# Optimization experiments

Measured on AMD Instinct MI355X. Metric: run time of the kernel, lower is better.

The kernel has to match this reference:

```python
import jax, jax.numpy as jnp
import numpy as np

N_NODES = 50000
N_EDGES = 800000
DIMS = [128, 512, 256, 128]
EPS = 1e-5


def setup_inputs() -> dict:
    key = jax.random.key(0)
    ks = jax.random.split(key, 2 + 5 * 3)
    inp = {
        "x": jax.random.normal(ks[0], (N_NODES, DIMS[0]), dtype=jnp.float32),
        "edge_index": jax.random.randint(ks[1], (2, N_EDGES), 0, N_NODES, dtype=jnp.int64),
    }
    ki = 2
    for i in range(3):
        din, dout = DIMS[i], DIMS[i + 1]
        s = 1.0 / np.sqrt(din)
        inp[f"Wl{i}"] = jax.random.uniform(ks[ki + 0], (din, dout), jnp.float32, -s, s)
        inp[f"bl{i}"] = jax.random.uniform(ks[ki + 1], (dout,), jnp.float32, -s, s)
        inp[f"Wr{i}"] = jax.random.uniform(ks[ki + 2], (din, dout), jnp.float32, -s, s)
        inp[f"g{i}"] = jnp.ones((dout,), jnp.float32)
        inp[f"b{i}"] = jnp.zeros((dout,), jnp.float32)
        ki += 5
    return inp


def _sage_mean(x, src, dst, Wl, bl, Wr):
    n = x.shape[0]
    agg = jax.ops.segment_sum(x[src], dst, num_segments=n)  # [N, din]
    deg = jax.ops.segment_sum(jnp.ones((src.shape[0],), x.dtype), dst, num_segments=n)
    mean = agg / jnp.maximum(deg, 1.0)[:, None]
    return mean @ Wl + bl + x @ Wr


def _bn(h, gamma, beta):
    m = h.mean(axis=0)
    v = h.var(axis=0)
    return gamma * (h - m) * jax.lax.rsqrt(v + EPS) + beta


def reference(x, edge_index, Wl0, bl0, Wr0, g0, b0, Wl1, bl1, Wr1, g1, b1, Wl2, bl2, Wr2, g2, b2):
    src, dst = edge_index[0], edge_index[1]
    params = [(Wl0, bl0, Wr0, g0, b0), (Wl1, bl1, Wr1, g1, b1), (Wl2, bl2, Wr2, g2, b2)]
    h = x
    for Wl, bl, Wr, g, b in params:
        h = _sage_mean(h, src, dst, Wl, bl, Wr)
        h = _bn(h, g, b)
        h = jax.nn.relu(h)
        # dropout: identity in eval mode
    return h
```

## Files before the change

### kernel.cpp

```cpp
#include <hip/hip_runtime.h>
#include <cstdint>
#include <cstddef>


#define EPS_BN 1e-5f

typedef unsigned short ushort_t;
typedef __attribute__((ext_vector_type(8))) short short8;
typedef __attribute__((ext_vector_type(4))) float float4v;
typedef __attribute__((ext_vector_type(2))) float float2v;
typedef __attribute__((ext_vector_type(2))) unsigned int uint2v;
typedef __attribute__((ext_vector_type(4))) unsigned int uint4v;

__device__ __forceinline__ float bflo(unsigned int w) {
    union { unsigned int i; float f; } v; v.i = w << 16; return v.f;
}
__device__ __forceinline__ float bfhi(unsigned int w) {
    union { unsigned int i; float f; } v; v.i = w & 0xffff0000u; return v.f;
}
__device__ __forceinline__ ushort_t f2bf(float f) {
    union { float f; unsigned int i; } v; v.f = f;
    unsigned int r = v.i + 0x7fffu + ((v.i >> 16) & 1u);
    return (ushort_t)(r >> 16);
}

__device__ __forceinline__ void async_copy16(void* lds, const void* g) {
    __builtin_amdgcn_global_load_lds(
        (const __attribute__((address_space(1))) unsigned int*)g,
        (__attribute__((address_space(3))) unsigned int*)lds, 16, 0, 0);
}

__device__ __forceinline__ void edge_sd(const int* __restrict__ p, int e, int ne,
                                        bool is64, int& s, int& d) {
    if (is64) { s = p[2 * e];  d = p[2 * ne + 2 * e]; }
    else      { s = p[e];      d = p[ne + e]; }
}
__device__ __forceinline__ int edge_d(const int* __restrict__ p, int e, int ne, bool is64) {
    return is64 ? p[2 * ne + 2 * e] : p[ne + e];
}

__device__ __forceinline__ bool detect_is64(const int* __restrict__ edges,
                                            int* sh_flag, int t) {
    if (t == 0) *sh_flag = 1;
    __syncthreads();
    if (t < 64 && edges[2 * t + 1] != 0) *sh_flag = 0;
    __syncthreads();
    return *sh_flag != 0;
}

#define EPB 2048

__global__ __launch_bounds__(256) void bhist_kernel(
    const int* __restrict__ edges, int ne, int* __restrict__ gcnt) {
    __shared__ int h[256];
    __shared__ int f64;
    int t = threadIdx.x;
    bool is64 = detect_is64(edges, &f64, t);
    h[t] = 0;
    __syncthreads();
    int base_e = blockIdx.x * EPB;
    #pragma unroll
    for (int u = 0; u < EPB / 256; ++u) {
        int i = base_e + u * 256 + t;
        if (i < ne) atomicAdd(&h[edge_d(edges, i, ne, is64) >> 8], 1);
    }
    __syncthreads();
    if (h[t]) atomicAdd(&gcnt[t], h[t]);
}

__global__ __launch_bounds__(256) void bscan_kernel(
    const int* __restrict__ gcnt, int nb, int ne,
    int* __restrict__ bbase, int* __restrict__ bcur) {
    __shared__ int sh[256];
    int t = threadIdx.x;
    int v = (t < nb) ? gcnt[t] : 0;
    sh[t] = v;
    __syncthreads();
    for (int o = 1; o < 256; o <<= 1) {
        int x = (t >= o) ? sh[t - o] : 0;
        __syncthreads();
        sh[t] += x;
        __syncthreads();
    }
    int excl = sh[t] - v;
    if (t < nb) { bbase[t] = excl; bcur[t] = excl; }
    if (t == nb) bbase[t] = ne;
    if (t == 0 && nb == 256) bbase[256] = ne;
}

__global__ __launch_bounds__(256) void bscatter_kernel(
    const int* __restrict__ edges, int ne,
    int* __restrict__ bcur, int* __restrict__ packed) {
    __shared__ int h[256];
    __shared__ int chunkb[256];
    __shared__ int lcur[256];
    __shared__ int f64;
    int t = threadIdx.x;
    bool is64 = detect_is64(edges, &f64, t);
    h[t] = 0;
    lcur[t] = 0;
    __syncthreads();
    int base_e = blockIdx.x * EPB;
    int ent[EPB / 256], eb[EPB / 256];
    #pragma unroll
    for (int u = 0; u < EPB / 256; ++u) {
        int i = base_e + u * 256 + t;
        if (i < ne) {
            int s, d;
            edge_sd(edges, i, ne, is64, s, d);
            ent[u] = s | ((d & 255) << 24);
            eb[u] = d >> 8;
            atomicAdd(&h[eb[u]], 1);
        } else eb[u] = -1;
    }
    __syncthreads();
    if (h[t]) chunkb[t] = atomicAdd(&bcur[t], h[t]);
    __syncthreads();
    #pragma unroll
    for (int u = 0; u < EPB / 256; ++u) {
        if (eb[u] >= 0) {
            int lp = atomicAdd(&lcur[eb[u]], 1);
            packed[chunkb[eb[u]] + lp] = ent[u];
        }
    }
}

__global__ __launch_bounds__(256) void bbuild_kernel(
    const int* __restrict__ packed, const int* __restrict__ bbase,
    int* __restrict__ rowptr, int* __restrict__ csr_src, int n) {
    __shared__ int h[256];
    __shared__ int cur[256];
    int t = threadIdx.x;
    int bb = blockIdx.x;
    int base = bbase[bb], cnt = bbase[bb + 1] - base;
    h[t] = 0;
    __syncthreads();
    for (int i = t; i < cnt; i += 256)
        atomicAdd(&h[(unsigned)packed[base + i] >> 24], 1);
    __syncthreads();
    int v = h[t];
    for (int o = 1; o < 256; o <<= 1) {
        int x = (t >= o) ? h[t - o] : 0;
        __syncthreads();
        h[t] += x;
        __syncthreads();
    }
    int excl = h[t] - v;
    int node = bb * 256 + t;
    if (node <= n) rowptr[node] = base + excl;
    cur[t] = excl;
    __syncthreads();
    for (int i = t; i < cnt; i += 256) {
        int e = packed[base + i];
        int lp = atomicAdd(&cur[(unsigned)e >> 24], 1);
        csr_src[base + lp] = e & 0xffffff;
    }
}

__global__ void prep_all_kernel(
    const float* __restrict__ x, ushort_t* __restrict__ xb, int nxb,
    const float* __restrict__ Wl0, const float* __restrict__ Wr0,
    ushort_t* __restrict__ WT0, int nb0,
    const float* __restrict__ Wl1, const float* __restrict__ Wr1,
    ushort_t* __restrict__ WT1c, int nb1,
    const float* __restrict__ Wl2, const float* __restrict__ Wr2,
    ushort_t* __restrict__ WT2c) {
    const int D0 = 128, D1 = 512, D2 = 256, D3 = 128;
    int b = blockIdx.x;
    if (b < nxb) {
        int i = b * 256 + threadIdx.x;
        xb[i] = f2bf(x[i]);
        return;
    }
    b -= nxb;
    if (b < nb0) {
        int idx = b * 256 + threadIdx.x;
        int K2 = 2 * D0;
        int nn = idx / K2, k = idx - nn * K2;
        float v = (k < D0) ? Wl0[(size_t)k * D1 + nn] : Wr0[(size_t)(k - D0) * D1 + nn];
        WT0[idx] = f2bf(v);
        return;
    }
    b -= nb0;
    if (b < nb1) {
        int idx = b * 256 + threadIdx.x;
        int nn = idx / D1, k = idx - nn * D1;
        float v = (nn < D2) ? Wl1[(size_t)k * D2 + nn] : Wr1[(size_t)k * D2 + (nn - D2)];
        WT1c[idx] = f2bf(v);
        return;
    }
    b -= nb1;
    {
        int idx = b * 256 + threadIdx.x;
        int nn = idx / D2, k = idx - nn * D2;
        float v = (nn < D3) ? Wl2[(size_t)k * D3 + nn] : Wr2[(size_t)k * D3 + (nn - D3)];
        WT2c[idx] = f2bf(v);
    }
}

template <int VEC> struct VecT;
template <> struct VecT<2> { using T = unsigned int; };
template <> struct VecT<4> { using T = uint2v; };
template <> struct VecT<8> { using T = uint4v; };

template <int VEC>
__device__ __forceinline__ void vunpack(typename VecT<VEC>::T v, unsigned int* w) {
    if constexpr (VEC == 2) { w[0] = v; }
    else if constexpr (VEC == 4) { w[0] = v.x; w[1] = v.y; }
    else { w[0] = v.x; w[1] = v.y; w[2] = v.z; w[3] = v.w; }
}

template <int VEC>
__device__ __forceinline__ void vaccum(typename VecT<VEC>::T v, float* acc) {
    unsigned int w[VEC / 2];
    vunpack<VEC>(v, w);
    #pragma unroll
    for (int i = 0; i < VEC / 2; ++i) {
        acc[2 * i + 0] += bflo(w[i]);
        acc[2 * i + 1] += bfhi(w[i]);
    }
}

template <int VEC>
__device__ __forceinline__ void gather_sum(
    const ushort_t* __restrict__ base, const int* __restrict__ csr_src,
    int e0, int e1, int rstride, float* acc) {
    using VT = typename VecT<VEC>::T;
    int e = e0;
    for (; e + 16 <= e1; e += 16) {
        VT v[16];
        #pragma unroll
        for (int u = 0; u < 16; ++u)
            v[u] = *(const VT*)(base + (size_t)csr_src[e + u] * rstride);
        #pragma unroll
        for (int u = 0; u < 16; ++u) vaccum<VEC>(v[u], acc);
    }
    if (e + 8 <= e1) {
        VT v[8];
        #pragma unroll
        for (int u = 0; u < 8; ++u)
            v[u] = *(const VT*)(base + (size_t)csr_src[e + u] * rstride);
        #pragma unroll
        for (int u = 0; u < 8; ++u) vaccum<VEC>(v[u], acc);
        e += 8;
    }
    if (e + 4 <= e1) {
        VT v[4];
        #pragma unroll
        for (int u = 0; u < 4; ++u)
            v[u] = *(const VT*)(base + (size_t)csr_src[e + u] * rstride);
        #pragma unroll
        for (int u = 0; u < 4; ++u) vaccum<VEC>(v[u], acc);
        e += 4;
    }
    if (e + 2 <= e1) {
        VT v0 = *(const VT*)(base + (size_t)csr_src[e] * rstride);
        VT v1 = *(const VT*)(base + (size_t)csr_src[e + 1] * rstride);
        vaccum<VEC>(v0, acc); vaccum<VEC>(v1, acc);
        e += 2;
    }
    if (e < e1)
        vaccum<VEC>(*(const VT*)(base + (size_t)csr_src[e] * rstride), acc);
}

template <int VEC>
__global__ __launch_bounds__(256) void aggregate_wave_kernel(
    const ushort_t* __restrict__ h, ushort_t* __restrict__ mean,
    const int* __restrict__ rowptr, const int* __restrict__ csr_src, int nnodes) {
    const int din = VEC * 64;
    const int wave = threadIdx.x >> 6;
    const int lane = threadIdx.x & 63;
    const int wstride = gridDim.x * 4;
    using VT = typename VecT<VEC>::T;
    for (int wid = blockIdx.x * 4 + wave; wid < nnodes; wid += wstride) {
        int e0 = rowptr[wid], e1 = rowptr[wid + 1];
        float acc[VEC];
        #pragma unroll
        for (int i = 0; i < VEC; ++i) acc[i] = 0.f;
        gather_sum<VEC>(h + (size_t)lane * VEC, csr_src, e0, e1, din, acc);

        int deg = e1 - e0;
        float scale = 1.0f / (float)(deg > 1 ? deg : 1);
        unsigned int o[VEC / 2];
        #pragma unroll
        for (int i = 0; i < VEC / 2; ++i)
            o[i] = (unsigned int)f2bf(acc[2 * i] * scale) |
                   ((unsigned int)f2bf(acc[2 * i + 1] * scale) << 16);
        VT ov;
        if constexpr (VEC == 2) { ov = o[0]; }
        else if constexpr (VEC == 4) { ov.x = o[0]; ov.y = o[1]; }
        else { ov.x = o[0]; ov.y = o[1]; ov.z = o[2]; ov.w = o[3]; }
        *(VT*)(mean + (size_t)wid * din + (size_t)lane * VEC) = ov;
    }
}

template <int VEC>
__global__ __launch_bounds__(256) void aggregate_add_kernel(
    const ushort_t* __restrict__ PR, const float* __restrict__ bias,
    ushort_t* __restrict__ pre,
    const int* __restrict__ rowptr, const int* __restrict__ csr_src, int nnodes,
    float* __restrict__ gsum, float* __restrict__ gsq) {
    const int D = VEC * 64;
    const int stride = 2 * D;
    __shared__ float s_red[2][4][VEC * 64];
    const int wave = threadIdx.x >> 6;
    const int lane = threadIdx.x & 63;
    const int wstride = gridDim.x * 4;
    using VT = typename VecT<VEC>::T;

    float ssum[VEC], ssq[VEC];
    #pragma unroll
    for (int i = 0; i < VEC; ++i) { ssum[i] = 0.f; ssq[i] = 0.f; }

    for (int wid = blockIdx.x * 4 + wave; wid < nnodes; wid += wstride) {
        int e0 = rowptr[wid], e1 = rowptr[wid + 1];
        float acc[VEC];
        #pragma unroll
        for (int i = 0; i < VEC; ++i) acc[i] = 0.f;
        gather_sum<VEC>(PR + (size_t)lane * VEC, csr_src, e0, e1, stride, acc);

        int deg = e1 - e0;
        float scale = 1.0f / (float)(deg > 1 ? deg : 1);

        VT rv = *(const VT*)(PR + (size_t)wid * stride + D + (size_t)lane * VEC);
        unsigned int rw[VEC / 2];
        vunpack<VEC>(rv, rw);
        float o[VEC];
        #pragma unroll
        for (int i = 0; i < VEC / 2; ++i) {
            o[2 * i + 0] = bflo(rw[i]);
            o[2 * i + 1] = bfhi(rw[i]);
        }
        #pragma unroll
        for (int i = 0; i < VEC; ++i) {
            o[i] += acc[i] * scale + bias[lane * VEC + i];
            ssum[i] += o[i];
            ssq[i] += o[i] * o[i];
        }

        unsigned int ow[VEC / 2];
        #pragma unroll
        for (int i = 0; i < VEC / 2; ++i)
            ow[i] = (unsigned int)f2bf(o[2 * i]) | ((unsigned int)f2bf(o[2 * i + 1]) << 16);
        VT ov;
        if constexpr (VEC == 2) { ov = ow[0]; }
        else if constexpr (VEC == 4) { ov.x = ow[0]; ov.y = ow[1]; }
        else { ov.x = ow[0]; ov.y = ow[1]; ov.z = ow[2]; ov.w = ow[3]; }
        *(VT*)(pre + (size_t)wid * D + (size_t)lane * VEC) = ov;
    }

    #pragma unroll
    for (int i = 0; i < VEC; ++i) {
        s_red[0][wave][lane * VEC + i] = ssum[i];
        s_red[1][wave][lane * VEC + i] = ssq[i];
    }
    __syncthreads();
    int t = threadIdx.x;
    if (t < D) {
        float a = s_red[0][0][t] + s_red[0][1][t] + s_red[0][2][t] + s_red[0][3][t];
        float q = s_red[1][0][t] + s_red[1][1][t] + s_red[1][2][t] + s_red[1][3][t];
        atomicAdd(&gsum[t], a);
        atomicAdd(&gsq[t], q);
    }
}

template <int K, int COLS, bool DUAL, bool BIAS, bool STATS>
__global__ __launch_bounds__(256, 2) void gemm_bres_kernel(
    const ushort_t* __restrict__ A1, const ushort_t* __restrict__ A2,
    const ushort_t* __restrict__ BT, const float* __restrict__ bias,
    ushort_t* __restrict__ Cb, int N, int nRowTiles, int RG, int panelsLog2,
    int Wtot, float* __restrict__ gsum, float* __restrict__ gsq) {
    __shared__ ushort_t Bs[COLS * K];

    const int tid = threadIdx.x;
    const int wave = tid >> 6;
    const int lane = tid & 63;
    const int quad = lane >> 4;
    const int l15 = lane & 15;

    const int nwg = gridDim.x;
    const int q = nwg >> 3, rr = nwg & 7;
    const int o = blockIdx.x;
    const int xcd = o & 7, sub = o >> 3;
    const int wgid = (xcd < rr ? xcd * (q + 1) : rr * (q + 1) + (xcd - rr) * q) + sub;
    const int panel = wgid & ((1 << panelsLog2) - 1);
    const int rowGroup = wgid >> panelsLog2;
    const int colBase = panel * COLS;

    constexpr int CPC = K / 8;
    constexpr int CPT = COLS * CPC / 256;
    #pragma unroll
    for (int u = 0; u < CPT; ++u) {
        int c = u * 256 + tid;
        int col = c / CPC, cc = c - col * CPC;
        int scc = cc ^ (col & 7);
        async_copy16(&Bs[c * 8], BT + (size_t)(colBase + col) * K + scc * 8);
    }
    __syncthreads();

    const int wm = (wave >> 1) * 64;
    constexpr int WN = COLS / 2;
    const int wn = (wave & 1) * WN;
    constexpr int NJ = WN / 16;
    constexpr int NKK = K / 32;
    constexpr int AS = DUAL ? K / 2 : K;

    float cs[NJ][4], cq[NJ][4];
    if constexpr (STATS) {
        #pragma unroll
        for (int j = 0; j < NJ; ++j)
            #pragma unroll
            for (int r = 0; r < 4; ++r) { cs[j][r] = 0.f; cq[j][r] = 0.f; }
    }

    for (int rt = rowGroup; rt < nRowTiles; rt += RG) {
        const int rowBase = rt * 128;
        const ushort_t* ap[4];
        const ushort_t* ap2[4];
        int growv[4];
        #pragma unroll
        for (int i = 0; i < 4; ++i) {
            int grow = rowBase + wm + i * 16 + l15;
            growv[i] = grow;
            if (grow >= N) grow = N - 1;
            ap[i] = A1 + (size_t)grow * AS + quad * 8;
            if (DUAL) ap2[i] = A2 + (size_t)grow * AS + quad * 8;
        }

        float4v acc[4][NJ];
        #pragma unroll
        for (int i = 0; i < 4; ++i)
            #pragma unroll
            for (int j = 0; j < NJ; ++j)
                acc[i][j] = (float4v){0.f, 0.f, 0.f, 0.f};

        #pragma unroll
        for (int kk = 0; kk < NKK; ++kk) {
            short8 af[4], bf[NJ];
            #pragma unroll
            for (int i = 0; i < 4; ++i) {
                if constexpr (DUAL) {
                    if (kk < NKK / 2) af[i] = *(const short8*)(ap[i] + kk * 32);
                    else              af[i] = *(const short8*)(ap2[i] + (kk - NKK / 2) * 32);
                } else {
                    af[i] = *(const short8*)(ap[i] + kk * 32);
                }
            }
            #pragma unroll
            for (int j = 0; j < NJ; ++j) {
                int col = wn + j * 16 + l15;
                int ct = (kk * 4 + quad) ^ (col & 7);
                bf[j] = *(const short8*)&Bs[col * K + ct * 8];
            }
            __builtin_amdgcn_s_setprio(1);
            #pragma unroll
            for (int i = 0; i < 4; ++i)
                #pragma unroll
                for (int j = 0; j < NJ; ++j)
                    acc[i][j] = __builtin_amdgcn_mfma_f32_16x16x32_bf16(bf[j], af[i], acc[i][j], 0, 0, 0);
            __builtin_amdgcn_s_setprio(0);
        }

        #pragma unroll
        for (int j = 0; j < NJ; ++j) {
            float4 bv = make_float4(0.f, 0.f, 0.f, 0.f);
            if (BIAS) bv = *(const float4*)(bias + colBase + wn + j * 16 + quad * 4);
            #pragma unroll
            for (int i = 0; i < 4; ++i) {
                float v0 = acc[i][j][0] + bv.x;
                float v1 = acc[i][j][1] + bv.y;
                float v2 = acc[i][j][2] + bv.z;
                float v3 = acc[i][j][3] + bv.w;
                if (growv[i] < N) {
                    if constexpr (STATS) {
                        cs[j][0] += v0; cq[j][0] += v0 * v0;
                        cs[j][1] += v1; cq[j][1] += v1 * v1;
                        cs[j][2] += v2; cq[j][2] += v2 * v2;
                        cs[j][3] += v3; cq[j][3] += v3 * v3;
                    }
                    uint2v pk;
                    pk.x = (unsigned int)f2bf(v0) | ((unsigned int)f2bf(v1) << 16);
                    pk.y = (unsigned int)f2bf(v2) | ((unsigned int)f2bf(v3) << 16);
                    *(uint2v*)(Cb + (size_t)growv[i] * Wtot + colBase + wn + j * 16 + quad * 4) = pk;
                }
            }
        }
    }

    if constexpr (STATS) {
        #pragma unroll
        for (int j = 0; j < NJ; ++j)
            #pragma unroll
            for (int r = 0; r < 4; ++r) {
                #pragma unroll
                for (int m = 1; m < 16; m <<= 1) {
                    cs[j][r] += __shfl_xor(cs[j][r], m);
                    cq[j][r] += __shfl_xor(cq[j][r], m);
                }
            }
        if (l15 == 0) {
            #pragma unroll
            for (int j = 0; j < NJ; ++j)
                #pragma unroll
                for (int r = 0; r < 4; ++r) {
                    int col = colBase + wn + j * 16 + quad * 4 + r;
                    atomicAdd(&gsum[col], cs[j][r]);
                    atomicAdd(&gsq[col], cq[j][r]);
                }
        }
    }
}

__global__ void bn_relu_b2b_kernel(const ushort_t* __restrict__ h, ushort_t* __restrict__ hb,
                                   int N, int D,
                                   const float* __restrict__ sum, const float* __restrict__ sumsq,
                                   const float* __restrict__ g, const float* __restrict__ b) {
    size_t idx = (size_t)blockIdx.x * blockDim.x + threadIdx.x;
    size_t tot = (size_t)N * D / 2;
    if (idx >= tot) return;
    int cp = (int)(idx & (size_t)(D / 2 - 1));
    int c0 = cp * 2, c1 = c0 + 1;
    float m0 = sum[c0] / (float)N, m1 = sum[c1] / (float)N;
    float i0 = rsqrtf(sumsq[c0] / (float)N - m0 * m0 + EPS_BN);
    float i1 = rsqrtf(sumsq[c1] / (float)N - m1 * m1 + EPS_BN);
    unsigned int w = ((const unsigned int*)h)[idx];
    float v0 = g[c0] * (bflo(w) - m0) * i0 + b[c0];
    float v1 = g[c1] * (bfhi(w) - m1) * i1 + b[c1];
    v0 = v0 > 0.f ? v0 : 0.f;
    v1 = v1 > 0.f ? v1 : 0.f;
    ((unsigned int*)hb)[idx] = (unsigned int)f2bf(v0) | ((unsigned int)f2bf(v1) << 16);
}

__global__ void bn_relu_b2f_kernel(const ushort_t* __restrict__ h, float* __restrict__ hf,
                                   int N, int D,
                                   const float* __restrict__ sum, const float* __restrict__ sumsq,
                                   const float* __restrict__ g, const float* __restrict__ b) {
    size_t idx = (size_t)blockIdx.x * blockDim.x + threadIdx.x;
    size_t tot = (size_t)N * D / 2;
    if (idx >= tot) return;
    int cp = (int)(idx & (size_t)(D / 2 - 1));
    int c0 = cp * 2, c1 = c0 + 1;
    float m0 = sum[c0] / (float)N, m1 = sum[c1] / (float)N;
    float i0 = rsqrtf(sumsq[c0] / (float)N - m0 * m0 + EPS_BN);
    float i1 = rsqrtf(sumsq[c1] / (float)N - m1 * m1 + EPS_BN);
    unsigned int w = ((const unsigned int*)h)[idx];
    float v0 = g[c0] * (bflo(w) - m0) * i0 + b[c0];
    float v1 = g[c1] * (bfhi(w) - m1) * i1 + b[c1];
    float2v o;
    o.x = v0 > 0.f ? v0 : 0.f;
    o.y = v1 > 0.f ? v1 : 0.f;
    *(float2v*)(hf + idx * 2) = o;
}

extern "C" void kernel_launch(void* const* d_in, const int* in_sizes, int n_in,
                              void* d_out, int out_size, void* d_ws, size_t ws_size,
                              hipStream_t stream) {
    const float* x     = (const float*)d_in[0];
    const int*   edges = (const int*)d_in[1];
    const float* Wl0 = (const float*)d_in[2];
    const float* bl0 = (const float*)d_in[3];
    const float* Wr0 = (const float*)d_in[4];
    const float* g0  = (const float*)d_in[5];
    const float* b0  = (const float*)d_in[6];
    const float* Wl1 = (const float*)d_in[7];
    const float* bl1 = (const float*)d_in[8];
    const float* Wr1 = (const float*)d_in[9];
    const float* g1  = (const float*)d_in[10];
    const float* b1  = (const float*)d_in[11];
    const float* Wl2 = (const float*)d_in[12];
    const float* bl2 = (const float*)d_in[13];
    const float* Wr2 = (const float*)d_in[14];
    const float* g2  = (const float*)d_in[15];
    const float* b2  = (const float*)d_in[16];

    const int D0 = 128, D1 = 512, D2 = 256, D3 = 128;
    const int n  = in_sizes[0] / D0;
    const int ne = in_sizes[1] / 2;
    const int NB = (n + 255) >> 8;

    char* base = (char*)d_ws;
    size_t off = 0;
    auto alloc = [&](size_t bytes) -> char* {
        char* p = base + off;
        off = (off + bytes + 255) & ~(size_t)255;
        return p;
    };
    int*      gcnt    = (int*)alloc(256 * 4);
    float*    stats   = (float*)alloc(6 * 512 * 4);
    size_t    zero_span = off;
    int*      bbase   = (int*)alloc(257 * 4);
    int*      bcur    = (int*)alloc(256 * 4);
    int*      packed  = (int*)alloc((size_t)ne * 4);
    int*      rowptr  = (int*)alloc((size_t)(n + 1) * 4);
    int*      csr_src = (int*)alloc((size_t)ne * 4);
    ushort_t* xb      = (ushort_t*)alloc((size_t)n * D0 * 2);
    ushort_t* mb      = (ushort_t*)alloc((size_t)n * 512 * 2);
    ushort_t* h1b     = (ushort_t*)alloc((size_t)n * D1 * 2);
    ushort_t* h2b     = (ushort_t*)alloc((size_t)n * D2 * 2);
    ushort_t* hpre    = (ushort_t*)alloc((size_t)n * 512 * 2);
    ushort_t* WT0     = (ushort_t*)alloc((size_t)D1 * 2 * D0 * 2);
    ushort_t* WT1c    = (ushort_t*)alloc((size_t)(2 * D2) * D1 * 2);
    ushort_t* WT2c    = (ushort_t*)alloc((size_t)(2 * D3) * D2 * 2);
    float*    out     = (float*)d_out;
    (void)ws_size; (void)n_in; (void)out_size;

    hipMemsetAsync(base, 0, zero_span, stream);

    int ablk = (ne + EPB - 1) / EPB;
    bhist_kernel<<<ablk, 256, 0, stream>>>(edges, ne, gcnt);
    bscan_kernel<<<1, 256, 0, stream>>>(gcnt, NB, ne, bbase, bcur);
    bscatter_kernel<<<ablk, 256, 0, stream>>>(edges, ne, bcur, packed);
    bbuild_kernel<<<NB, 256, 0, stream>>>(packed, bbase, rowptr, csr_src, n);

    const int nxb = (n * D0) / 256;
    const int nb0 = (D1 * 2 * D0) / 256;
    const int nb1 = (2 * D2 * D1) / 256;
    const int nb2 = (2 * D3 * D2) / 256;
    prep_all_kernel<<<nxb + nb0 + nb1 + nb2, 256, 0, stream>>>(
        x, xb, nxb, Wl0, Wr0, WT0, nb0, Wl1, Wr1, WT1c, nb1, Wl2, Wr2, WT2c);

    const int aggGrid = 2048;
    const int rowTiles = (n + 127) / 128;
    float* st0 = stats + 0 * 1024;
    float* st1 = stats + 1 * 1024;
    float* st2 = stats + 2 * 1024;

    aggregate_wave_kernel<2><<<aggGrid, 256, 0, stream>>>(xb, mb, rowptr, csr_src, n);
    gemm_bres_kernel<256, 128, true, true, true><<<512, 256, 0, stream>>>(
        mb, xb, WT0, bl0, hpre, n, rowTiles, 128, 2, D1, st0, st0 + 512);
    bn_relu_b2b_kernel<<<((size_t)n * D1 / 2 + 255) / 256, 256, 0, stream>>>(
        hpre, h1b, n, D1, st0, st0 + 512, g0, b0);

    gemm_bres_kernel<512, 64, false, false, false><<<512, 256, 0, stream>>>(
        h1b, nullptr, WT1c, nullptr, mb, n, rowTiles, 64, 3, 2 * D2, nullptr, nullptr);
    aggregate_add_kernel<4><<<aggGrid, 256, 0, stream>>>(
        mb, bl1, hpre, rowptr, csr_src, n, st1, st1 + 512);
    bn_relu_b2b_kernel<<<((size_t)n * D2 / 2 + 255) / 256, 256, 0, stream>>>(
        hpre, h2b, n, D2, st1, st1 + 512, g1, b1);

    gemm_bres_kernel<256, 128, false, false, false><<<512, 256, 0, stream>>>(
        h2b, nullptr, WT2c, nullptr, mb, n, rowTiles, 256, 1, 2 * D3, nullptr, nullptr);
    aggregate_add_kernel<2><<<aggGrid, 256, 0, stream>>>(
        mb, bl2, hpre, rowptr, csr_src, n, st2, st2 + 512);
    bn_relu_b2f_kernel<<<((size_t)n * D3 / 2 + 255) / 256, 256, 0, stream>>>(
        hpre, out, n, D3, st2, st2 + 512, g2, b2);
}
```

Before: 604.7 us.

## Retile bf16 GEMM into 512-thread blocks with 32x32 per-wave tiles

Reworks the GEMM so each of 8 waves computes a 32x32 output tile. Column panels become narrower (32 or 64 columns) and row tiles become 128 or 256 rows. Grids grow to roughly 800-1000 workgroups with launch bounds asking for 6 blocks per CU, and the s_setprio hints around the MFMA block are removed. The aim is more parallelism and occupancy with a smaller LDS footprint per block. The cost is less register-level reuse per wave, and A rows are re-read from global memory once per extra column panel.

```diff
diff --git a/kernel.cpp b/kernel.cpp
--- a/kernel.cpp
+++ b/kernel.cpp
@@ -364,12 +364,14 @@
     }
 }
 
-template <int K, int COLS, bool DUAL, bool BIAS, bool STATS>
-__global__ __launch_bounds__(256, 2) void gemm_bres_kernel(
+template <int K, int ROWW, int COLW, bool DUAL, bool BIAS, bool STATS>
+__global__ __launch_bounds__(512, 6) void gemm_bres_kernel(
     const ushort_t* __restrict__ A1, const ushort_t* __restrict__ A2,
     const ushort_t* __restrict__ BT, const float* __restrict__ bias,
     ushort_t* __restrict__ Cb, int N, int nRowTiles, int RG, int panelsLog2,
     int Wtot, float* __restrict__ gsum, float* __restrict__ gsq) {
+    constexpr int COLS = COLW * 32;
+    constexpr int BR = ROWW * 32;
     __shared__ ushort_t Bs[COLS * K];
 
     const int tid = threadIdx.x;
@@ -377,6 +379,8 @@
     const int lane = tid & 63;
     const int quad = lane >> 4;
     const int l15 = lane & 15;
+    const int wr = wave / COLW;
+    const int wc = wave % COLW;
 
     const int nwg = gridDim.x;
     const int q = nwg >> 3, rr = nwg & 7;
@@ -388,57 +392,53 @@
     const int colBase = panel * COLS;
 
     constexpr int CPC = K / 8;
-    constexpr int CPT = COLS * CPC / 256;
+    constexpr int CPT = COLS * CPC / 512;
     #pragma unroll
     for (int u = 0; u < CPT; ++u) {
-        int c = u * 256 + tid;
+        int c = u * 512 + tid;
         int col = c / CPC, cc = c - col * CPC;
         int scc = cc ^ (col & 7);
         async_copy16(&Bs[c * 8], BT + (size_t)(colBase + col) * K + scc * 8);
     }
     __syncthreads();
 
-    const int wm = (wave >> 1) * 64;
-    constexpr int WN = COLS / 2;
-    const int wn = (wave & 1) * WN;
-    constexpr int NJ = WN / 16;
     constexpr int NKK = K / 32;
     constexpr int AS = DUAL ? K / 2 : K;
 
-    float cs[NJ][4], cq[NJ][4];
+    float cs[2][4], cq[2][4];
     if constexpr (STATS) {
         #pragma unroll
-        for (int j = 0; j < NJ; ++j)
+        for (int j = 0; j < 2; ++j)
             #pragma unroll
             for (int r = 0; r < 4; ++r) { cs[j][r] = 0.f; cq[j][r] = 0.f; }
     }
 
     for (int rt = rowGroup; rt < nRowTiles; rt += RG) {
-        const int rowBase = rt * 128;
-        const ushort_t* ap[4];
-        const ushort_t* ap2[4];
-        int growv[4];
-        #pragma unroll
-        for (int i = 0; i < 4; ++i) {
-            int grow = rowBase + wm + i * 16 + l15;
+        const int rowBase = rt * BR;
+        const ushort_t* ap[2];
+        const ushort_t* ap2[2];
+        int growv[2];
+        #pragma unroll
+        for (int i = 0; i < 2; ++i) {
+            int grow = rowBase + wr * 32 + i * 16 + l15;
             growv[i] = grow;
             if (grow >= N) grow = N - 1;
             ap[i] = A1 + (size_t)grow * AS + quad * 8;
             if (DUAL) ap2[i] = A2 + (size_t)grow * AS + quad * 8;
         }
 
-        float4v acc[4][NJ];
-        #pragma unroll
-        for (int i = 0; i < 4; ++i)
-            #pragma unroll
-            for (int j = 0; j < NJ; ++j)
+        float4v acc[2][2];
+        #pragma unroll
+        for (int i = 0; i < 2; ++i)
+            #pragma unroll
+            for (int j = 0; j < 2; ++j)
                 acc[i][j] = (float4v){0.f, 0.f, 0.f, 0.f};
 
         #pragma unroll
         for (int kk = 0; kk < NKK; ++kk) {
-            short8 af[4], bf[NJ];
-            #pragma unroll
-            for (int i = 0; i < 4; ++i) {
+            short8 af[2], bf[2];
+            #pragma unroll
+            for (int i = 0; i < 2; ++i) {
                 if constexpr (DUAL) {
                     if (kk < NKK / 2) af[i] = *(const short8*)(ap[i] + kk * 32);
                     else              af[i] = *(const short8*)(ap2[i] + (kk - NKK / 2) * 32);
@@ -447,26 +447,24 @@
                 }
             }
             #pragma unroll
-            for (int j = 0; j < NJ; ++j) {
-                int col = wn + j * 16 + l15;
+            for (int j = 0; j < 2; ++j) {
+                int col = wc * 32 + j * 16 + l15;
                 int ct = (kk * 4 + quad) ^ (col & 7);
                 bf[j] = *(const short8*)&Bs[col * K + ct * 8];
             }
-            __builtin_amdgcn_s_setprio(1);
-            #pragma unroll
-            for (int i = 0; i < 4; ++i)
+            #pragma unroll
+            for (int i = 0; i < 2; ++i)
                 #pragma unroll
-                for (int j = 0; j < NJ; ++j)
+                for (int j = 0; j < 2; ++j)
                     acc[i][j] = __builtin_amdgcn_mfma_f32_16x16x32_bf16(bf[j], af[i], acc[i][j], 0, 0, 0);
-            __builtin_amdgcn_s_setprio(0);
         }
 
         #pragma unroll
-        for (int j = 0; j < NJ; ++j) {
+        for (int j = 0; j < 2; ++j) {
             float4 bv = make_float4(0.f, 0.f, 0.f, 0.f);
-            if (BIAS) bv = *(const float4*)(bias + colBase + wn + j * 16 + quad * 4);
-            #pragma unroll
-            for (int i = 0; i < 4; ++i) {
+            if (BIAS) bv = *(const float4*)(bias + colBase + wc * 32 + j * 16 + quad * 4);
+            #pragma unroll
+            for (int i = 0; i < 2; ++i) {
                 float v0 = acc[i][j][0] + bv.x;
                 float v1 = acc[i][j][1] + bv.y;
                 float v2 = acc[i][j][2] + bv.z;
@@ -481,7 +479,7 @@
                     uint2v pk;
                     pk.x = (unsigned int)f2bf(v0) | ((unsigned int)f2bf(v1) << 16);
                     pk.y = (unsigned int)f2bf(v2) | ((unsigned int)f2bf(v3) << 16);
-                    *(uint2v*)(Cb + (size_t)growv[i] * Wtot + colBase + wn + j * 16 + quad * 4) = pk;
+                    *(uint2v*)(Cb + (size_t)growv[i] * Wtot + colBase + wc * 32 + j * 16 + quad * 4) = pk;
                 }
             }
         }
@@ -489,7 +487,7 @@
 
     if constexpr (STATS) {
         #pragma unroll
-        for (int j = 0; j < NJ; ++j)
+        for (int j = 0; j < 2; ++j)
             #pragma unroll
             for (int r = 0; r < 4; ++r) {
                 #pragma unroll
@@ -500,10 +498,10 @@
             }
         if (l15 == 0) {
             #pragma unroll
-            for (int j = 0; j < NJ; ++j)
+            for (int j = 0; j < 2; ++j)
                 #pragma unroll
                 for (int r = 0; r < 4; ++r) {
-                    int col = colBase + wn + j * 16 + quad * 4 + r;
+                    int col = colBase + wc * 32 + j * 16 + quad * 4 + r;
                     atomicAdd(&gsum[col], cs[j][r]);
                     atomicAdd(&gsq[col], cq[j][r]);
                 }
@@ -620,26 +618,27 @@
         x, xb, nxb, Wl0, Wr0, WT0, nb0, Wl1, Wr1, WT1c, nb1, Wl2, Wr2, WT2c);
 
     const int aggGrid = 2048;
-    const int rowTiles = (n + 127) / 128;
+    const int rowTiles128 = (n + 127) / 128;
+    const int rowTiles256 = (n + 255) / 256;
     float* st0 = stats + 0 * 1024;
     float* st1 = stats + 1 * 1024;
     float* st2 = stats + 2 * 1024;
 
     aggregate_wave_kernel<2><<<aggGrid, 256, 0, stream>>>(xb, mb, rowptr, csr_src, n);
-    gemm_bres_kernel<256, 128, true, true, true><<<512, 256, 0, stream>>>(
-        mb, xb, WT0, bl0, hpre, n, rowTiles, 128, 2, D1, st0, st0 + 512);
+    gemm_bres_kernel<256, 4, 2, true, true, true><<<1048, 512, 0, stream>>>(
+        mb, xb, WT0, bl0, hpre, n, rowTiles128, 131, 3, D1, st0, st0 + 512);
     bn_relu_b2b_kernel<<<((size_t)n * D1 / 2 + 255) / 256, 256, 0, stream>>>(
         hpre, h1b, n, D1, st0, st0 + 512, g0, b0);
 
-    gemm_bres_kernel<512, 64, false, false, false><<<512, 256, 0, stream>>>(
-        h1b, nullptr, WT1c, nullptr, mb, n, rowTiles, 64, 3, 2 * D2, nullptr, nullptr);
+    gemm_bres_kernel<512, 8, 1, false, false, false><<<784, 512, 0, stream>>>(
+        h1b, nullptr, WT1c, nullptr, mb, n, rowTiles256, 49, 4, 2 * D2, nullptr, nullptr);
     aggregate_add_kernel<4><<<aggGrid, 256, 0, stream>>>(
         mb, bl1, hpre, rowptr, csr_src, n, st1, st1 + 512);
     bn_relu_b2b_kernel<<<((size_t)n * D2 / 2 + 255) / 256, 256, 0, stream>>>(
         hpre, h2b, n, D2, st1, st1 + 512, g1, b1);
 
-    gemm_bres_kernel<256, 128, false, false, false><<<512, 256, 0, stream>>>(
-        h2b, nullptr, WT2c, nullptr, mb, n, rowTiles, 256, 1, 2 * D3, nullptr, nullptr);
+    gemm_bres_kernel<256, 4, 2, false, false, false><<<784, 512, 0, stream>>>(
+        h2b, nullptr, WT2c, nullptr, mb, n, rowTiles128, 196, 2, 2 * D3, nullptr, nullptr);
     aggregate_add_kernel<2><<<aggGrid, 256, 0, stream>>>(
         mb, bl2, hpre, rowptr, csr_src, n, st2, st2 + 512);
     bn_relu_b2f_kernel<<<((size_t)n * D3 / 2 + 255) / 256, 256, 0, stream>>>(
```

Measured after the change: 874.5 us. 1.45x slower.
